# Kernel optimization log

Hardware: AMD Instinct MI355X
Metric: run time of the kernel (lower is better)

Reference implementation:

```python
import jax, jax.numpy as jnp
import numpy as np

M, N, DV, DC, ITERS = 512, 1024, 3, 6, 10
BATCH = 8192
ATANH_CLIP = 0.999995


def _build_graph():
    """Deterministic (3,6)-regular Tanner graph, edge order = row-major nonzeros of H."""
    offsets = [0, 1, 2, 512, 515, 519]
    H = np.zeros((M, N), np.int64)
    r = np.arange(M)
    for off in offsets:
        H[r, (2 * r + off) % N] = 1
    ei, ej = np.nonzero(H)                       # E = M*DC = 3072 edges, row-major
    E = ei.size
    var2edges = np.argsort(ej, kind='stable').reshape(N, DV)   # edges of each variable
    chk2edges = np.argsort(ei, kind='stable').reshape(M, DC)   # edges of each check
    v_sum = np.empty((E, DV - 1), np.int64)      # for edge e: other edges on same variable
    c_prod = np.empty((E, DC - 1), np.int64)     # for edge e: other edges on same check
    for e in range(E):
        gv = var2edges[ej[e]]
        v_sum[e] = gv[gv != e]
        gc = chk2edges[ei[e]]
        c_prod[e] = gc[gc != e]
    return v_sum, c_prod, ej.astype(np.int64), var2edges


def setup_inputs() -> dict:
    key = jax.random.key(0)
    ks = jax.random.split(key, 6)
    v_sum, c_prod, edge_var, var2edges = _build_graph()
    E = edge_var.shape[0]                        # 3072
    TW = E * (DV - 1)                            # total_weights = 6144
    return {
        "llr": jax.random.normal(ks[0], (BATCH, N), jnp.float32),
        "w_iter": 1.0 + 0.1 * jax.random.normal(ks[1], (ITERS, TW), jnp.float32),
        "llr_iter": 1.0 + 0.1 * jax.random.normal(ks[2], (ITERS, N), jnp.float32),
        "w_final": 1.0 + 0.1 * jax.random.normal(ks[3], (E,), jnp.float32),
        "llr_final": 1.0 + 0.1 * jax.random.normal(ks[4], (N,), jnp.float32),
        "v_sum_idx": jnp.asarray(v_sum),         # [E, DV-1]
        "c_prod_idx": jnp.asarray(c_prod),       # [E, DC-1]
        "edge_var": jnp.asarray(edge_var),       # [E] variable index of each edge
        "final_idx": jnp.asarray(var2edges),     # [N, DV] edges feeding each variable marginal
    }


def reference(llr, w_iter, llr_iter, w_final, llr_final,
              v_sum_idx, c_prod_idx, edge_var, final_idx):
    B = llr.shape[0]
    E = edge_var.shape[0]
    c2v0 = jnp.zeros((B, E), llr.dtype)

    def bp_iter(c2v, params):
        w, lw = params                                      # [E*(DV-1)], [N]
        # variable -> check: weighted sum of extrinsic c2v messages + weighted LLR
        s = (c2v[:, v_sum_idx] * w.reshape(E, DV - 1)).sum(-1)        # [B,E]
        v2c = jnp.tanh(0.5 * (s + (llr * lw)[:, edge_var]))           # [B,E]
        # check -> variable: product of extrinsic v2c messages, 2*atanh
        prods = v2c[:, c_prod_idx].prod(-1)                           # [B,E]
        return 2.0 * jnp.arctanh(ATANH_CLIP * prods), None

    c2v, _ = jax.lax.scan(bp_iter, c2v0, (w_iter, llr_iter))
    # final marginalization: per-variable sum of weighted incoming messages
    fin = (c2v[:, final_idx.reshape(-1)] * w_final).reshape(B, N, DV).sum(-1)
    out = fin + llr * llr_final
    return jax.nn.sigmoid(out[:, : N - M])
```

## Files before the change

### kernel.cpp

```cpp
#include <hip/hip_runtime.h>


namespace {

typedef float v4f __attribute__((ext_vector_type(4)));

constexpr int T      = 512;
constexpr int ROWS   = 4;
constexpr int EEDG   = 3072;
constexpr int NVAR   = 1024;
constexpr int NITER  = 10;
constexpr int BATCH  = 8192;
constexpr int NOUT   = 512;

constexpr float LOG2E = 1.4426950408889634f;
constexpr float LN2   = 0.6931471805599453f;
constexpr float KAPPA = 0.999995f;
constexpr float ACLMP = 24.0f;

__device__ __forceinline__ float fast_exp2(float x) { return __builtin_amdgcn_exp2f(x); }
__device__ __forceinline__ float fast_log2(float x) { return __builtin_amdgcn_logf(x); }
__device__ __forceinline__ float fast_rcp (float x) { return __builtin_amdgcn_rcpf(x); }

__device__ __forceinline__ int swz(int s) {
    return (s & ~31) | ((s >> 1) & 15) | ((s & 1) << 4);
}

__global__ __launch_bounds__(T, 1)
void bp_decode(const float* __restrict__ llr,
               const float* __restrict__ w_iter,
               const float* __restrict__ llr_iter,
               const float* __restrict__ w_final,
               const float* __restrict__ llr_final,
               const int*  __restrict__ v_sum_idx,
               const int*  __restrict__ edge_var,
               const int*  __restrict__ final_idx,
               float* __restrict__ out)
{
    __shared__ v4f Ad[2 * EEDG];

    const int  tid = threadIdx.x;
    const long b0  = (long)blockIdx.x * ROWS;

    #pragma unroll
    for (int k = 0; k < 6; ++k)
        Ad[k * T + tid] = (v4f)(0.f);

    int nb[12];
    int own[6];
    int var[6];
    v4f Lpre[6];
    {
        const int4* p = (const int4*)(v_sum_idx + 12 * tid);
        int4 q0 = p[0], q1 = p[1], q2 = p[2];
        nb[0]  = swz(q0.x); nb[1]  = swz(q0.y); nb[2]  = swz(q0.z); nb[3]  = swz(q0.w);
        nb[4]  = swz(q1.x); nb[5]  = swz(q1.y); nb[6]  = swz(q1.z); nb[7]  = swz(q1.w);
        nb[8]  = swz(q2.x); nb[9]  = swz(q2.y); nb[10] = swz(q2.z); nb[11] = swz(q2.w);
    }
    #pragma unroll
    for (int j = 0; j < 6; ++j) own[j] = swz(6 * tid + j);
    {
        const int2* p = (const int2*)(edge_var + 6 * tid);
        int2 q0 = p[0], q1 = p[1], q2 = p[2];
        var[0]=q0.x; var[1]=q0.y; var[2]=q1.x; var[3]=q1.y; var[4]=q2.x; var[5]=q2.y;
        #pragma unroll
        for (int j = 0; j < 6; ++j) {
            v4f L;
            L.x = llr[(b0 + 0) * NVAR + var[j]];
            L.y = llr[(b0 + 1) * NVAR + var[j]];
            L.z = llr[(b0 + 2) * NVAR + var[j]];
            L.w = llr[(b0 + 3) * NVAR + var[j]];
            Lpre[j] = L * LOG2E;
        }
    }

    float w[12], lv[6];
    {
        const float* p = w_iter + 12 * tid;
        float4 a = ((const float4*)p)[0], b = ((const float4*)p)[1], c = ((const float4*)p)[2];
        w[0]=a.x; w[1]=a.y; w[2]=a.z;  w[3]=a.w;
        w[4]=b.x; w[5]=b.y; w[6]=b.z;  w[7]=b.w;
        w[8]=c.x; w[9]=c.y; w[10]=c.z; w[11]=c.w;
        #pragma unroll
        for (int j = 0; j < 6; ++j) lv[j] = llr_iter[var[j]];
    }

    __syncthreads();

#define BP_ITER(IT, RDOFF, WROFF) do {                                          \
        v4f a_[6];                                                              \
        _Pragma("unroll")                                                       \
        for (int j = 0; j < 6; ++j) a_[j] = Lpre[j] * lv[j];                    \
        _Pragma("unroll")                                                       \
        for (int i = 0; i < 6; ++i) {                                           \
            v4f ga = Ad[nb[2*i]   + (RDOFF)];                 \
            v4f gb = Ad[nb[2*i+1] + (RDOFF)];                                   \
            a_[i] = a_[i] + w[2*i] * ga + w[2*i+1] * gb;                        \
        }                                                                       \
             \
        const int itn_ = ((IT) + 1 < NITER) ? (IT) + 1 : (IT);                  \
        const float* pw_ = w_iter + (long)itn_ * (EEDG * 2) + 12 * tid;         \
        float4 qa_ = ((const float4*)pw_)[0];                                   \
        float4 qb_ = ((const float4*)pw_)[1];                                   \
        float4 qc_ = ((const float4*)pw_)[2];                                   \
        const float* lit_ = llr_iter + itn_ * NVAR;                             \
        float lvn_[6];                                                          \
        _Pragma("unroll")                                                       \
        for (int j = 0; j < 6; ++j) lvn_[j] = lit_[var[j]];                     \
                                                     \
        v4f zm_[6], zp_[6];                                                     \
        _Pragma("unroll")                                                       \
        for (int j = 0; j < 6; ++j) {                                           \
            v4f aa = __builtin_elementwise_min(a_[j], (v4f)(ACLMP));            \
            v4f z;                                                              \
            z.x = fast_exp2(aa.x);                                              \
            z.y = fast_exp2(aa.y);                                              \
            z.z = fast_exp2(aa.z);                                              \
            z.w = fast_exp2(aa.w);                                              \
            zm_[j] = z - 1.f;                                                   \
            zp_[j] = z + 1.f;                                                   \
        }                                                                       \
        v4f A_[6], B_[6];                                                       \
        {                                                                       \
            v4f P1=zm_[0], P2=P1*zm_[1], P3=P2*zm_[2], P4=P3*zm_[3], P5=P4*zm_[4]; \
            v4f S4=zm_[5], S3=S4*zm_[4], S2=S3*zm_[3], S1=S2*zm_[2], S0=S1*zm_[1]; \
            A_[0]=S0; A_[1]=P1*S1; A_[2]=P2*S2; A_[3]=P3*S3; A_[4]=P4*S4; A_[5]=P5; \
        }                                                                       \
        {                                                                       \
            v4f P1=zp_[0], P2=P1*zp_[1], P3=P2*zp_[2], P4=P3*zp_[3], P5=P4*zp_[4]; \
            v4f S4=zp_[5], S3=S4*zp_[4], S2=S3*zp_[3], S1=S2*zp_[2], S0=S1*zp_[1]; \
            B_[0]=S0; B_[1]=P1*S1; B_[2]=P2*S2; B_[3]=P3*S3; B_[4]=P4*S4; B_[5]=P5; \
        }                                                                       \
        _Pragma("unroll")                                                       \
        for (int j = 0; j < 6; ++j) {                                           \
            v4f num = KAPPA * A_[j] + B_[j];                        \
            v4f den = B_[j] - KAPPA * A_[j];                        \
            v4f d;                                                              \
            d.x = fast_log2(num.x) - fast_log2(den.x);                          \
            d.y = fast_log2(num.y) - fast_log2(den.y);                          \
            d.z = fast_log2(num.z) - fast_log2(den.z);                          \
            d.w = fast_log2(num.w) - fast_log2(den.w);                          \
            Ad[own[j] + (WROFF)] = d;                        \
        }                                                                       \
                                     \
        w[0]=qa_.x; w[1]=qa_.y; w[2]=qa_.z;  w[3]=qa_.w;                        \
        w[4]=qb_.x; w[5]=qb_.y; w[6]=qb_.z;  w[7]=qb_.w;                        \
        w[8]=qc_.x; w[9]=qc_.y; w[10]=qc_.z; w[11]=qc_.w;                       \
        _Pragma("unroll")                                                       \
        for (int j = 0; j < 6; ++j) lv[j] = lvn_[j];                            \
        __syncthreads();                                                        \
    } while (0)

    for (int it = 0; it < NITER; it += 2) {
        BP_ITER(it,     0,    EEDG);
        BP_ITER(it + 1, EEDG, 0);
    }
#undef BP_ITER

    {
        int f0 = swz(final_idx[3*tid]), f1 = swz(final_idx[3*tid + 1]), f2 = swz(final_idx[3*tid + 2]);
        v4f d0 = Ad[f0];
        v4f d1 = Ad[f1];
        v4f d2 = Ad[f2];
        float wf0 = w_final[3*tid], wf1 = w_final[3*tid + 1], wf2 = w_final[3*tid + 2];
        float lf  = llr_final[tid];
        v4f l;
        l.x = llr[(b0 + 0) * NVAR + tid];
        l.y = llr[(b0 + 1) * NVAR + tid];
        l.z = llr[(b0 + 2) * NVAR + tid];
        l.w = llr[(b0 + 3) * NVAR + tid];

        v4f fin = (d0 * wf0 + d1 * wf1 + d2 * wf2) * LN2;
        v4f v   = l * lf + fin;
        out[(b0 + 0) * NOUT + tid] = fast_rcp(1.f + fast_exp2(-v.x * LOG2E));
        out[(b0 + 1) * NOUT + tid] = fast_rcp(1.f + fast_exp2(-v.y * LOG2E));
        out[(b0 + 2) * NOUT + tid] = fast_rcp(1.f + fast_exp2(-v.z * LOG2E));
        out[(b0 + 3) * NOUT + tid] = fast_rcp(1.f + fast_exp2(-v.w * LOG2E));
    }
}

}

extern "C" void kernel_launch(void* const* d_in, const int* in_sizes, int n_in,
                              void* d_out, int out_size, void* d_ws, size_t ws_size,
                              hipStream_t stream)
{
    const float* llr       = (const float*)d_in[0];
    const float* w_iter    = (const float*)d_in[1];
    const float* llr_iter  = (const float*)d_in[2];
    const float* w_final   = (const float*)d_in[3];
    const float* llr_final = (const float*)d_in[4];
    const int*   v_sum_idx = (const int*)d_in[5];
    const int*   edge_var  = (const int*)d_in[7];
    const int*   final_idx = (const int*)d_in[8];
    float* outp = (float*)d_out;

    dim3 grid(BATCH / ROWS), block(T);
    hipLaunchKernelGGL(bp_decode, grid, block, 0, stream,
                       llr, w_iter, llr_iter, w_final, llr_final,
                       v_sum_idx, edge_var, final_idx, outp);
}
```

Measured before the change: 236.3 us.

## Single-buffer shared messages, pack indices, loop row groups per persistent block

Measured after the change: 330.1 us. +39.7%, slower.

```diff
diff --git a/kernel.cpp b/kernel.cpp
--- a/kernel.cpp
+++ b/kernel.cpp
@@ -7,6 +7,7 @@
 
 constexpr int T      = 512;
 constexpr int ROWS   = 4;
+constexpr int GROUPS = 4;
 constexpr int EEDG   = 3072;
 constexpr int NVAR   = 1024;
 constexpr int NITER  = 10;
@@ -26,7 +27,7 @@
     return (s & ~31) | ((s >> 1) & 15) | ((s & 1) << 4);
 }
 
-__global__ __launch_bounds__(T, 1)
+__global__ __launch_bounds__(T, 4)
 void bp_decode(const float* __restrict__ llr,
                const float* __restrict__ w_iter,
                const float* __restrict__ llr_iter,
@@ -37,68 +38,33 @@
                const int*  __restrict__ final_idx,
                float* __restrict__ out)
 {
-    __shared__ v4f Ad[2 * EEDG];
-
-    const int  tid = threadIdx.x;
-    const long b0  = (long)blockIdx.x * ROWS;
-
-    #pragma unroll
-    for (int k = 0; k < 6; ++k)
-        Ad[k * T + tid] = (v4f)(0.f);
-
-    int nb[12];
-    int own[6];
-    int var[6];
-    v4f Lpre[6];
+    __shared__ v4f Ad[EEDG];
+
+    const int tid = threadIdx.x;
+    const int own = 6 * tid;
+
+    unsigned nbp[6];
+    unsigned varp[3];
     {
         const int4* p = (const int4*)(v_sum_idx + 12 * tid);
         int4 q0 = p[0], q1 = p[1], q2 = p[2];
-        nb[0]  = swz(q0.x); nb[1]  = swz(q0.y); nb[2]  = swz(q0.z); nb[3]  = swz(q0.w);
-        nb[4]  = swz(q1.x); nb[5]  = swz(q1.y); nb[6]  = swz(q1.z); nb[7]  = swz(q1.w);
-        nb[8]  = swz(q2.x); nb[9]  = swz(q2.y); nb[10] = swz(q2.z); nb[11] = swz(q2.w);
+        nbp[0] = (unsigned)swz(q0.x) | ((unsigned)swz(q0.y) << 16);
+        nbp[1] = (unsigned)swz(q0.z) | ((unsigned)swz(q0.w) << 16);
+        nbp[2] = (unsigned)swz(q1.x) | ((unsigned)swz(q1.y) << 16);
+        nbp[3] = (unsigned)swz(q1.z) | ((unsigned)swz(q1.w) << 16);
+        nbp[4] = (unsigned)swz(q2.x) | ((unsigned)swz(q2.y) << 16);
+        nbp[5] = (unsigned)swz(q2.z) | ((unsigned)swz(q2.w) << 16);
     }
-    #pragma unroll
-    for (int j = 0; j < 6; ++j) own[j] = swz(6 * tid + j);
     {
         const int2* p = (const int2*)(edge_var + 6 * tid);
         int2 q0 = p[0], q1 = p[1], q2 = p[2];
-        var[0]=q0.x; var[1]=q0.y; var[2]=q1.x; var[3]=q1.y; var[4]=q2.x; var[5]=q2.y;
-        #pragma unroll
-        for (int j = 0; j < 6; ++j) {
-            v4f L;
-            L.x = llr[(b0 + 0) * NVAR + var[j]];
-            L.y = llr[(b0 + 1) * NVAR + var[j]];
-            L.z = llr[(b0 + 2) * NVAR + var[j]];
-            L.w = llr[(b0 + 3) * NVAR + var[j]];
-            Lpre[j] = L * LOG2E;
-        }
+        varp[0] = (unsigned)q0.x | ((unsigned)q0.y << 16);
+        varp[1] = (unsigned)q1.x | ((unsigned)q1.y << 16);
+        varp[2] = (unsigned)q2.x | ((unsigned)q2.y << 16);
     }
 
-    float w[12], lv[6];
-    {
-        const float* p = w_iter + 12 * tid;
-        float4 a = ((const float4*)p)[0], b = ((const float4*)p)[1], c = ((const float4*)p)[2];
-        w[0]=a.x; w[1]=a.y; w[2]=a.z;  w[3]=a.w;
-        w[4]=b.x; w[5]=b.y; w[6]=b.z;  w[7]=b.w;
-        w[8]=c.x; w[9]=c.y; w[10]=c.z; w[11]=c.w;
-        #pragma unroll
-        for (int j = 0; j < 6; ++j) lv[j] = llr_iter[var[j]];
-    }
-
-    __syncthreads();
-
-#define BP_ITER(IT, RDOFF, WROFF) do {                                          \
-        v4f a_[6];                                                              \
-        _Pragma("unroll")                                                       \
-        for (int j = 0; j < 6; ++j) a_[j] = Lpre[j] * lv[j];                    \
-        _Pragma("unroll")                                                       \
-        for (int i = 0; i < 6; ++i) {                                           \
-            v4f ga = Ad[nb[2*i]   + (RDOFF)];                 \
-            v4f gb = Ad[nb[2*i+1] + (RDOFF)];                                   \
-            a_[i] = a_[i] + w[2*i] * ga + w[2*i+1] * gb;                        \
-        }                                                                       \
-             \
-        const int itn_ = ((IT) + 1 < NITER) ? (IT) + 1 : (IT);                  \
+#define BP_TAIL(ITN) do {                                                       \
+        const int itn_ = (ITN);                                                 \
         const float* pw_ = w_iter + (long)itn_ * (EEDG * 2) + 12 * tid;         \
         float4 qa_ = ((const float4*)pw_)[0];                                   \
         float4 qb_ = ((const float4*)pw_)[1];                                   \
@@ -106,12 +72,15 @@
         const float* lit_ = llr_iter + itn_ * NVAR;                             \
         float lvn_[6];                                                          \
         _Pragma("unroll")                                                       \
-        for (int j = 0; j < 6; ++j) lvn_[j] = lit_[var[j]];                     \
-                                                     \
+        for (int i = 0; i < 3; ++i) {                                           \
+            unsigned q = varp[i];                                               \
+            lvn_[2*i]   = lit_[q & 0xffffu];                                    \
+            lvn_[2*i+1] = lit_[q >> 16];                                        \
+        }                                                                       \
         v4f zm_[6], zp_[6];                                                     \
         _Pragma("unroll")                                                       \
         for (int j = 0; j < 6; ++j) {                                           \
-            v4f aa = __builtin_elementwise_min(a_[j], (v4f)(ACLMP));            \
+            v4f aa = __builtin_elementwise_min(a[j], (v4f)(ACLMP));             \
             v4f z;                                                              \
             z.x = fast_exp2(aa.x);                                              \
             z.y = fast_exp2(aa.y);                                              \
@@ -140,43 +109,98 @@
             d.y = fast_log2(num.y) - fast_log2(den.y);                          \
             d.z = fast_log2(num.z) - fast_log2(den.z);                          \
             d.w = fast_log2(num.w) - fast_log2(den.w);                          \
-            Ad[own[j] + (WROFF)] = d;                        \
-        }                                                                       \
-                                     \
+            Ad[swz(own + j)] = d;                \
+        }                                                                       \
         w[0]=qa_.x; w[1]=qa_.y; w[2]=qa_.z;  w[3]=qa_.w;                        \
         w[4]=qb_.x; w[5]=qb_.y; w[6]=qb_.z;  w[7]=qb_.w;                        \
         w[8]=qc_.x; w[9]=qc_.y; w[10]=qc_.z; w[11]=qc_.w;                       \
         _Pragma("unroll")                                                       \
         for (int j = 0; j < 6; ++j) lv[j] = lvn_[j];                            \
-        __syncthreads();                                                        \
     } while (0)
 
-    for (int it = 0; it < NITER; it += 2) {
-        BP_ITER(it,     0,    EEDG);
-        BP_ITER(it + 1, EEDG, 0);
+    for (int g = 0; g < GROUPS; ++g) {
+        const long b0 = ((long)blockIdx.x * GROUPS + g) * ROWS;
+
+        v4f Lpre[6];
+        #pragma unroll
+        for (int i = 0; i < 3; ++i) {
+            unsigned q = varp[i];
+            int v0 = q & 0xffffu, v1 = q >> 16;
+            v4f L0, L1;
+            L0.x = llr[(b0 + 0) * NVAR + v0];
+            L0.y = llr[(b0 + 1) * NVAR + v0];
+            L0.z = llr[(b0 + 2) * NVAR + v0];
+            L0.w = llr[(b0 + 3) * NVAR + v0];
+            L1.x = llr[(b0 + 0) * NVAR + v1];
+            L1.y = llr[(b0 + 1) * NVAR + v1];
+            L1.z = llr[(b0 + 2) * NVAR + v1];
+            L1.w = llr[(b0 + 3) * NVAR + v1];
+            Lpre[2*i]   = L0 * LOG2E;
+            Lpre[2*i+1] = L1 * LOG2E;
+        }
+        float w[12], lv[6];
+        {
+            const float* p = w_iter + 12 * tid;
+            float4 a4 = ((const float4*)p)[0], b4 = ((const float4*)p)[1], c4 = ((const float4*)p)[2];
+            w[0]=a4.x; w[1]=a4.y; w[2]=a4.z;  w[3]=a4.w;
+            w[4]=b4.x; w[5]=b4.y; w[6]=b4.z;  w[7]=b4.w;
+            w[8]=c4.x; w[9]=c4.y; w[10]=c4.z; w[11]=c4.w;
+            #pragma unroll
+            for (int i = 0; i < 3; ++i) {
+                unsigned q = varp[i];
+                lv[2*i]   = llr_iter[q & 0xffffu];
+                lv[2*i+1] = llr_iter[q >> 16];
+            }
+        }
+
+        {
+            v4f a[6];
+            #pragma unroll
+            for (int j = 0; j < 6; ++j) a[j] = Lpre[j] * lv[j];
+            __syncthreads();
+            BP_TAIL(1);
+            __syncthreads();
+        }
+
+        #pragma unroll 3
+        for (int it = 1; it < NITER; ++it) {
+            v4f a[6];
+            #pragma unroll
+            for (int j = 0; j < 6; ++j) a[j] = Lpre[j] * lv[j];
+            #pragma unroll
+            for (int i = 0; i < 6; ++i) {
+                unsigned p  = nbp[i];
+                v4f ga = Ad[p & 0xffffu];
+                v4f gb = Ad[p >> 16];
+                a[i] = a[i] + w[2*i] * ga + w[2*i+1] * gb;
+            }
+            __syncthreads();
+            BP_TAIL((it + 1 < NITER) ? it + 1 : it);
+            __syncthreads();
+        }
+
+        {
+            int f0 = swz(final_idx[3*tid]), f1 = swz(final_idx[3*tid + 1]), f2 = swz(final_idx[3*tid + 2]);
+            v4f d0 = Ad[f0];
+            v4f d1 = Ad[f1];
+            v4f d2 = Ad[f2];
+            float wf0 = w_final[3*tid], wf1 = w_final[3*tid + 1], wf2 = w_final[3*tid + 2];
+            float lf  = llr_final[tid];
+            v4f l;
+            l.x = llr[(b0 + 0) * NVAR + tid];
+            l.y = llr[(b0 + 1) * NVAR + tid];
+            l.z = llr[(b0 + 2) * NVAR + tid];
+            l.w = llr[(b0 + 3) * NVAR + tid];
+
+            v4f fin = (d0 * wf0 + d1 * wf1 + d2 * wf2) * LN2;
+            v4f v   = l * lf + fin;
+            out[(b0 + 0) * NOUT + tid] = fast_rcp(1.f + fast_exp2(-v.x * LOG2E));
+            out[(b0 + 1) * NOUT + tid] = fast_rcp(1.f + fast_exp2(-v.y * LOG2E));
+            out[(b0 + 2) * NOUT + tid] = fast_rcp(1.f + fast_exp2(-v.z * LOG2E));
+            out[(b0 + 3) * NOUT + tid] = fast_rcp(1.f + fast_exp2(-v.w * LOG2E));
+        }
     }
-#undef BP_ITER
-
-    {
-        int f0 = swz(final_idx[3*tid]), f1 = swz(final_idx[3*tid + 1]), f2 = swz(final_idx[3*tid + 2]);
-        v4f d0 = Ad[f0];
-        v4f d1 = Ad[f1];
-        v4f d2 = Ad[f2];
-        float wf0 = w_final[3*tid], wf1 = w_final[3*tid + 1], wf2 = w_final[3*tid + 2];
-        float lf  = llr_final[tid];
-        v4f l;
-        l.x = llr[(b0 + 0) * NVAR + tid];
-        l.y = llr[(b0 + 1) * NVAR + tid];
-        l.z = llr[(b0 + 2) * NVAR + tid];
-        l.w = llr[(b0 + 3) * NVAR + tid];
-
-        v4f fin = (d0 * wf0 + d1 * wf1 + d2 * wf2) * LN2;
-        v4f v   = l * lf + fin;
-        out[(b0 + 0) * NOUT + tid] = fast_rcp(1.f + fast_exp2(-v.x * LOG2E));
-        out[(b0 + 1) * NOUT + tid] = fast_rcp(1.f + fast_exp2(-v.y * LOG2E));
-        out[(b0 + 2) * NOUT + tid] = fast_rcp(1.f + fast_exp2(-v.z * LOG2E));
-        out[(b0 + 3) * NOUT + tid] = fast_rcp(1.f + fast_exp2(-v.w * LOG2E));
-    }
+#undef BP_TAIL
 }
 
 }
@@ -195,7 +219,7 @@
     const int*   final_idx = (const int*)d_in[8];
     float* outp = (float*)d_out;
 
-    dim3 grid(BATCH / ROWS), block(T);
+    dim3 grid(BATCH / (ROWS * GROUPS)), block(T);
     hipLaunchKernelGGL(bp_decode, grid, block, 0, stream,
                        llr, w_iter, llr_iter, w_final, llr_final,
                        v_sum_idx, edge_var, final_idx, outp);
```
